# Kernel tuning notes

Hardware: AMD Instinct MI355X
Metric: run time of the kernel (lower is better)

Reference implementation:

```python
import jax, jax.numpy as jnp
import numpy as np


def setup_inputs() -> dict:
    key = jax.random.key(0)
    k1, k2 = jax.random.split(key)
    B, L = 8192, 4096
    v = jax.random.normal(k1, (B, L), dtype=jnp.float32)
    z = jax.random.normal(k2, (B, L), dtype=jnp.float32)
    return {"v": v, "z": z}


def reference(v, z):
    # Householder reflection: z_new = z - 2 * v (v . z) / ||v||^2
    # Mathematically identical to the original bmm(v v^T, z) formulation,
    # but contracts the rank-1 outer product analytically (no BxLxL tensor).
    vz = jnp.sum(v * z, axis=1, keepdims=True)        # [B, 1] = v . z per row
    norm_sq = jnp.sum(v * v, axis=1, keepdims=True)    # [B, 1] = ||v||^2
    return z - 2.0 * v * (vz / norm_sq)
```

## Files before the change

### kernel.cpp

```cpp
#include <hip/hip_runtime.h>


#define L_DIM 4096
#define BLOCK 256
#define WPB (BLOCK / 64)
#define NF4 (L_DIM / 4 / 64)

typedef float f4 __attribute__((ext_vector_type(4)));

__global__ __launch_bounds__(BLOCK, 3) void householder_kernel(
    const float* __restrict__ v,
    const float* __restrict__ z,
    float* __restrict__ out,
    int B)
{
    const int wave = threadIdx.x >> 6;
    const int lane = threadIdx.x & 63;
    const int row = blockIdx.x * WPB + wave;
    if (row >= B) return;

    const size_t base = (size_t)row * L_DIM;
    const f4* v4 = (const f4*)(v + base);
    const f4* z4 = (const f4*)(z + base);
    f4* o4 = (f4*)(out + base);

    f4 a[NF4], b[NF4];
    #pragma unroll
    for (int j = 0; j < NF4; ++j) {
        a[j] = v4[lane + j * 64];
        b[j] = z4[lane + j * 64];
    }

    float vz0 = 0.f, vz1 = 0.f, vz2 = 0.f, vz3 = 0.f;
    float vv0 = 0.f, vv1 = 0.f, vv2 = 0.f, vv3 = 0.f;
    #pragma unroll
    for (int j = 0; j < NF4; j += 4) {
        vz0 = fmaf(a[j+0].x, b[j+0].x, vz0); vz0 = fmaf(a[j+0].y, b[j+0].y, vz0);
        vz0 = fmaf(a[j+0].z, b[j+0].z, vz0); vz0 = fmaf(a[j+0].w, b[j+0].w, vz0);
        vv0 = fmaf(a[j+0].x, a[j+0].x, vv0); vv0 = fmaf(a[j+0].y, a[j+0].y, vv0);
        vv0 = fmaf(a[j+0].z, a[j+0].z, vv0); vv0 = fmaf(a[j+0].w, a[j+0].w, vv0);

        vz1 = fmaf(a[j+1].x, b[j+1].x, vz1); vz1 = fmaf(a[j+1].y, b[j+1].y, vz1);
        vz1 = fmaf(a[j+1].z, b[j+1].z, vz1); vz1 = fmaf(a[j+1].w, b[j+1].w, vz1);
        vv1 = fmaf(a[j+1].x, a[j+1].x, vv1); vv1 = fmaf(a[j+1].y, a[j+1].y, vv1);
        vv1 = fmaf(a[j+1].z, a[j+1].z, vv1); vv1 = fmaf(a[j+1].w, a[j+1].w, vv1);

        vz2 = fmaf(a[j+2].x, b[j+2].x, vz2); vz2 = fmaf(a[j+2].y, b[j+2].y, vz2);
        vz2 = fmaf(a[j+2].z, b[j+2].z, vz2); vz2 = fmaf(a[j+2].w, b[j+2].w, vz2);
        vv2 = fmaf(a[j+2].x, a[j+2].x, vv2); vv2 = fmaf(a[j+2].y, a[j+2].y, vv2);
        vv2 = fmaf(a[j+2].z, a[j+2].z, vv2); vv2 = fmaf(a[j+2].w, a[j+2].w, vv2);

        vz3 = fmaf(a[j+3].x, b[j+3].x, vz3); vz3 = fmaf(a[j+3].y, b[j+3].y, vz3);
        vz3 = fmaf(a[j+3].z, b[j+3].z, vz3); vz3 = fmaf(a[j+3].w, b[j+3].w, vz3);
        vv3 = fmaf(a[j+3].x, a[j+3].x, vv3); vv3 = fmaf(a[j+3].y, a[j+3].y, vv3);
        vv3 = fmaf(a[j+3].w, a[j+3].w, vv3); vv3 = fmaf(a[j+3].z, a[j+3].z, vv3);
    }
    float vz = (vz0 + vz1) + (vz2 + vz3);
    float vv = (vv0 + vv1) + (vv2 + vv3);

    #pragma unroll
    for (int off = 32; off > 0; off >>= 1) {
        vz += __shfl_xor(vz, off, 64);
        vv += __shfl_xor(vv, off, 64);
    }
    const float s = -2.0f * vz / vv;

    #pragma unroll
    for (int j = 0; j < NF4; ++j) {
        f4 r;
        r.x = fmaf(s, a[j].x, b[j].x);
        r.y = fmaf(s, a[j].y, b[j].y);
        r.z = fmaf(s, a[j].z, b[j].z);
        r.w = fmaf(s, a[j].w, b[j].w);
        o4[lane + j * 64] = r;
    }
}

extern "C" void kernel_launch(void* const* d_in, const int* in_sizes, int n_in,
                              void* d_out, int out_size, void* d_ws, size_t ws_size,
                              hipStream_t stream) {
    const float* v = (const float*)d_in[0];
    const float* z = (const float*)d_in[1];
    float* out = (float*)d_out;
    const int B = in_sizes[0] / L_DIM;
    const int grid = (B + WPB - 1) / WPB;
    householder_kernel<<<grid, BLOCK, 0, stream>>>(v, z, out, B);
}
```

Measured before the change: 311.1 us.

## Stream rows twice instead of holding them in registers to raise occupancy

The kernel no longer keeps each row's 16 float4 of v and z in registers. It does a first streaming pass for the dot products, then reloads v and z from memory for the output pass. Launch bounds go from 3 to 8 blocks per CU so the lower register use can hold more waves in flight. The trade is extra global or cache reads: each 16 KB row pair is read twice, and the second read may hit L2 or the MALL but may also go to HBM.

```diff
diff --git a/kernel.cpp b/kernel.cpp
--- a/kernel.cpp
+++ b/kernel.cpp
@@ -8,7 +8,7 @@
 
 typedef float f4 __attribute__((ext_vector_type(4)));
 
-__global__ __launch_bounds__(BLOCK, 3) void householder_kernel(
+__global__ __launch_bounds__(BLOCK, 8) void householder_kernel(
     const float* __restrict__ v,
     const float* __restrict__ z,
     float* __restrict__ out,
@@ -24,36 +24,33 @@
     const f4* z4 = (const f4*)(z + base);
     f4* o4 = (f4*)(out + base);
 
-    f4 a[NF4], b[NF4];
-    #pragma unroll
-    for (int j = 0; j < NF4; ++j) {
-        a[j] = v4[lane + j * 64];
-        b[j] = z4[lane + j * 64];
-    }
-
     float vz0 = 0.f, vz1 = 0.f, vz2 = 0.f, vz3 = 0.f;
     float vv0 = 0.f, vv1 = 0.f, vv2 = 0.f, vv3 = 0.f;
-    #pragma unroll
     for (int j = 0; j < NF4; j += 4) {
-        vz0 = fmaf(a[j+0].x, b[j+0].x, vz0); vz0 = fmaf(a[j+0].y, b[j+0].y, vz0);
-        vz0 = fmaf(a[j+0].z, b[j+0].z, vz0); vz0 = fmaf(a[j+0].w, b[j+0].w, vz0);
-        vv0 = fmaf(a[j+0].x, a[j+0].x, vv0); vv0 = fmaf(a[j+0].y, a[j+0].y, vv0);
-        vv0 = fmaf(a[j+0].z, a[j+0].z, vv0); vv0 = fmaf(a[j+0].w, a[j+0].w, vv0);
+        f4 a0 = v4[lane + (j+0)*64]; f4 b0 = z4[lane + (j+0)*64];
+        f4 a1 = v4[lane + (j+1)*64]; f4 b1 = z4[lane + (j+1)*64];
+        f4 a2 = v4[lane + (j+2)*64]; f4 b2 = z4[lane + (j+2)*64];
+        f4 a3 = v4[lane + (j+3)*64]; f4 b3 = z4[lane + (j+3)*64];
 
-        vz1 = fmaf(a[j+1].x, b[j+1].x, vz1); vz1 = fmaf(a[j+1].y, b[j+1].y, vz1);
-        vz1 = fmaf(a[j+1].z, b[j+1].z, vz1); vz1 = fmaf(a[j+1].w, b[j+1].w, vz1);
-        vv1 = fmaf(a[j+1].x, a[j+1].x, vv1); vv1 = fmaf(a[j+1].y, a[j+1].y, vv1);
-        vv1 = fmaf(a[j+1].z, a[j+1].z, vv1); vv1 = fmaf(a[j+1].w, a[j+1].w, vv1);
+        vz0 = fmaf(a0.x, b0.x, vz0); vz0 = fmaf(a0.y, b0.y, vz0);
+        vz0 = fmaf(a0.z, b0.z, vz0); vz0 = fmaf(a0.w, b0.w, vz0);
+        vv0 = fmaf(a0.x, a0.x, vv0); vv0 = fmaf(a0.y, a0.y, vv0);
+        vv0 = fmaf(a0.z, a0.z, vv0); vv0 = fmaf(a0.w, a0.w, vv0);
 
-        vz2 = fmaf(a[j+2].x, b[j+2].x, vz2); vz2 = fmaf(a[j+2].y, b[j+2].y, vz2);
-        vz2 = fmaf(a[j+2].z, b[j+2].z, vz2); vz2 = fmaf(a[j+2].w, b[j+2].w, vz2);
-        vv2 = fmaf(a[j+2].x, a[j+2].x, vv2); vv2 = fmaf(a[j+2].y, a[j+2].y, vv2);
-        vv2 = fmaf(a[j+2].z, a[j+2].z, vv2); vv2 = fmaf(a[j+2].w, a[j+2].w, vv2);
+        vz1 = fmaf(a1.x, b1.x, vz1); vz1 = fmaf(a1.y, b1.y, vz1);
+        vz1 = fmaf(a1.z, b1.z, vz1); vz1 = fmaf(a1.w, b1.w, vz1);
+        vv1 = fmaf(a1.x, a1.x, vv1); vv1 = fmaf(a1.y, a1.y, vv1);
+        vv1 = fmaf(a1.z, a1.z, vv1); vv1 = fmaf(a1.w, a1.w, vv1);
 
-        vz3 = fmaf(a[j+3].x, b[j+3].x, vz3); vz3 = fmaf(a[j+3].y, b[j+3].y, vz3);
-        vz3 = fmaf(a[j+3].z, b[j+3].z, vz3); vz3 = fmaf(a[j+3].w, b[j+3].w, vz3);
-        vv3 = fmaf(a[j+3].x, a[j+3].x, vv3); vv3 = fmaf(a[j+3].y, a[j+3].y, vv3);
-        vv3 = fmaf(a[j+3].w, a[j+3].w, vv3); vv3 = fmaf(a[j+3].z, a[j+3].z, vv3);
+        vz2 = fmaf(a2.x, b2.x, vz2); vz2 = fmaf(a2.y, b2.y, vz2);
+        vz2 = fmaf(a2.z, b2.z, vz2); vz2 = fmaf(a2.w, b2.w, vz2);
+        vv2 = fmaf(a2.x, a2.x, vv2); vv2 = fmaf(a2.y, a2.y, vv2);
+        vv2 = fmaf(a2.z, a2.z, vv2); vv2 = fmaf(a2.w, a2.w, vv2);
+
+        vz3 = fmaf(a3.x, b3.x, vz3); vz3 = fmaf(a3.y, b3.y, vz3);
+        vz3 = fmaf(a3.z, b3.z, vz3); vz3 = fmaf(a3.w, b3.w, vz3);
+        vv3 = fmaf(a3.x, a3.x, vv3); vv3 = fmaf(a3.y, a3.y, vv3);
+        vv3 = fmaf(a3.w, a3.w, vv3); vv3 = fmaf(a3.z, a3.z, vv3);
     }
     float vz = (vz0 + vz1) + (vz2 + vz3);
     float vv = (vv0 + vv1) + (vv2 + vv3);
@@ -65,14 +62,26 @@
     }
     const float s = -2.0f * vz / vv;
 
-    #pragma unroll
-    for (int j = 0; j < NF4; ++j) {
-        f4 r;
-        r.x = fmaf(s, a[j].x, b[j].x);
-        r.y = fmaf(s, a[j].y, b[j].y);
-        r.z = fmaf(s, a[j].z, b[j].z);
-        r.w = fmaf(s, a[j].w, b[j].w);
-        o4[lane + j * 64] = r;
+    for (int j = 0; j < NF4; j += 4) {
+        f4 a0 = v4[lane + (j+0)*64]; f4 b0 = z4[lane + (j+0)*64];
+        f4 a1 = v4[lane + (j+1)*64]; f4 b1 = z4[lane + (j+1)*64];
+        f4 a2 = v4[lane + (j+2)*64]; f4 b2 = z4[lane + (j+2)*64];
+        f4 a3 = v4[lane + (j+3)*64]; f4 b3 = z4[lane + (j+3)*64];
+
+        f4 r0, r1, r2, r3;
+        r0.x = fmaf(s, a0.x, b0.x); r0.y = fmaf(s, a0.y, b0.y);
+        r0.z = fmaf(s, a0.z, b0.z); r0.w = fmaf(s, a0.w, b0.w);
+        r1.x = fmaf(s, a1.x, b1.x); r1.y = fmaf(s, a1.y, b1.y);
+        r1.z = fmaf(s, a1.z, b1.z); r1.w = fmaf(s, a1.w, b1.w);
+        r2.x = fmaf(s, a2.x, b2.x); r2.y = fmaf(s, a2.y, b2.y);
+        r2.z = fmaf(s, a2.z, b2.z); r2.w = fmaf(s, a2.w, b2.w);
+        r3.x = fmaf(s, a3.x, b3.x); r3.y = fmaf(s, a3.y, b3.y);
+        r3.z = fmaf(s, a3.z, b3.z); r3.w = fmaf(s, a3.w, b3.w);
+
+        o4[lane + (j+0)*64] = r0;
+        o4[lane + (j+1)*64] = r1;
+        o4[lane + (j+2)*64] = r2;
+        o4[lane + (j+3)*64] = r3;
     }
 }
 
```

Measured after the change: 397.2 us. 27.7% more time.
